# Kernel tuning notes

Measured on AMD Instinct MI355X. Metric: run time of the kernel, lower is better.

## Reference

```python
import jax, jax.numpy as jnp
import numpy as np

DIM = 384
WIN = 64
HEADS = 12
B_ = 4096


def setup_inputs() -> dict:
    key = jax.random.key(0)
    k1, k2, k3, k4, k5 = jax.random.split(key, 5)
    x = jax.random.normal(k1, (B_, WIN, DIM), dtype=jnp.float32)
    # torch Linear weights: qkv.weight [3*dim, dim], proj.weight [dim, dim], proj.bias [dim]
    qkv_w = jax.random.normal(k2, (3 * DIM, DIM), dtype=jnp.float32) * (DIM ** -0.5)
    proj_w = jax.random.normal(k3, (DIM, DIM), dtype=jnp.float32) * (DIM ** -0.5)
    proj_b = jax.random.normal(k4, (DIM,), dtype=jnp.float32) * 0.02
    bias_table = jax.random.normal(k5, (2 * WIN - 1, HEADS), dtype=jnp.float32) * 0.02
    return {"x": x, "qkv_w": qkv_w, "proj_w": proj_w, "proj_b": proj_b,
            "bias_table": bias_table}


def reference(x, qkv_w, proj_w, proj_b, bias_table):
    B, N, C = x.shape
    H = HEADS
    hd = C // H
    scale = hd ** -0.5
    # qkv projection (torch: x @ W.T), split into q,k,v [B,H,N,hd]
    qkv = jnp.einsum('bnc,dc->bnd', x, qkv_w)
    qkv = qkv.reshape(B, N, 3, H, hd).transpose(2, 0, 3, 1, 4)
    q, k, v = qkv[0] * scale, qkv[1], qkv[2]
    attn = jnp.einsum('bhnd,bhmd->bhnm', q, k)  # [B,H,N,N]
    # relative position bias: index [N,N] into table [2W-1,H]
    coords = jnp.arange(N)
    rel_idx = coords[:, None] - coords[None, :] + (N - 1)  # [N,N]
    bias = bias_table[rel_idx]  # [N,N,H]
    attn = attn + bias.transpose(2, 0, 1)[None]
    attn = jax.nn.softmax(attn, axis=-1)
    out = jnp.einsum('bhnm,bhmd->bhnd', attn, v)
    out = out.transpose(0, 2, 1, 3).reshape(B, N, C)
    out = jnp.einsum('bnc,dc->bnd', out, proj_w) + proj_b
    return out
```

## Files before the change

kernel.cpp:

```cpp
#include <hip/hip_runtime.h>
#include <stdint.h>

#define DIM 384
#define WIN 64
#define HEADS 12
#define HD 32
#define NWIN 4096

typedef _Float16 f16;
typedef unsigned int u32;
typedef _Float16 half8 __attribute__((ext_vector_type(8)));
typedef _Float16 half4 __attribute__((ext_vector_type(4)));
typedef float floatx4 __attribute__((ext_vector_type(4)));

#define AS1 __attribute__((address_space(1)))
#define AS3 __attribute__((address_space(3)))

__device__ __forceinline__ void gl_lds16(const void* g, void* l) {
    __builtin_amdgcn_global_load_lds((const AS1 u32*)g, (AS3 u32*)l, 16, 0, 0);
}

__global__ void cvt_kernel(const float* __restrict__ in, f16* __restrict__ out, long n4) {
    long i = (long)blockIdx.x * blockDim.x + threadIdx.x;
    const long stride = (long)gridDim.x * blockDim.x;
    for (; i < n4; i += stride) {
        float4 v = ((const float4*)in)[i];
        half4 h;
        h[0] = (f16)v.x; h[1] = (f16)v.y; h[2] = (f16)v.z; h[3] = (f16)v.w;
        ((half4*)out)[i] = h;
    }
}

__global__ void pack_w_kernel(const float* __restrict__ w, f16* __restrict__ Bp) {
    const int t = blockIdx.x * 256 + threadIdx.x;
    const int colb = t / 9216;
    const int r1 = t % 9216;
    const int s = r1 / 768;
    const int r2 = r1 % 768;
    const int kc = r2 / 192, u = r2 % 192;
    const float* sp = w + (size_t)(colb * 192 + u) * DIM + s * 32 + kc * 8;
    float4 a = *(const float4*)sp;
    float4 b = *(const float4*)(sp + 4);
    half8 o;
    o[0] = (f16)a.x; o[1] = (f16)a.y; o[2] = (f16)a.z; o[3] = (f16)a.w;
    o[4] = (f16)b.x; o[5] = (f16)b.y; o[6] = (f16)b.z; o[7] = (f16)b.w;
    *(half8*)(Bp + (size_t)t * 8) = o;
}

__global__ void pack_x_kernel(const float* __restrict__ x, f16* __restrict__ Xp) {
    const int b = blockIdx.x;
    const int s = b % 12;
    const int rowb = b / 12;
    const int t = threadIdx.x;
    const int kc = t & 3, rr = t >> 2;
#pragma unroll
    for (int h = 0; h < 2; ++h) {
        const int row = rr + h * 64;
        const float* sp = x + (size_t)(rowb * 128 + row) * DIM + s * 32 + kc * 8;
        float4 a = *(const float4*)sp;
        float4 bq = *(const float4*)(sp + 4);
        half8 o;
        o[0] = (f16)a.x;  o[1] = (f16)a.y;  o[2] = (f16)a.z;  o[3] = (f16)a.w;
        o[4] = (f16)bq.x; o[5] = (f16)bq.y; o[6] = (f16)bq.z; o[7] = (f16)bq.w;
        *(half8*)(Xp + ((size_t)b * 512 + kc * 128 + row) * 8) = o;
    }
}

__global__ void __launch_bounds__(512, 2)
qkv_kernel(const f16* __restrict__ Xp, const f16* __restrict__ Bp,
           f16* __restrict__ q_arr, f16* __restrict__ k_arr,
           f16* __restrict__ v_int, int nwg)
{
    __shared__ __align__(16) f16 ldsA[2][16384];
    __shared__ __align__(16) f16 ldsB[3][12288];

    int lin = blockIdx.x;
    int nlin = lin;
    if ((nwg & 7) == 0) nlin = (lin & 7) * (nwg >> 3) + (lin >> 3);
    const int colb = nlin % 6, rowb = nlin / 6;

    const int tid = threadIdx.x;
    const int wave = tid >> 6, lane = tid & 63;
    const int g = lane >> 4, c = lane & 15;
    const int wm = wave >> 1, wn = wave & 1;

    floatx4 acc[4][6] = {};

    auto stageA = [&](int t) {
        f16* da = &ldsA[t & 1][0];
#pragma unroll
        for (int r = 0; r < 4; ++r) {
            const int rg = r >> 1, ss = r & 1;
            const f16* src = Xp + ((size_t)(2 * rowb + rg) * 12 + (2 * t + ss)) * 4096
                             + (size_t)tid * 8;
            gl_lds16(src, da + r * 4096 + tid * 8);
        }
    };
    auto stageB = [&](int t) {
        f16* db = &ldsB[t % 3][0];
#pragma unroll
        for (int r = 0; r < 3; ++r) {
            const int ch = r * 512 + tid;
            const int ss = ch / 768, rem = ch % 768;
            const f16* src = Bp + ((size_t)colb * 12 + (2 * t + ss)) * 6144 + (size_t)rem * 8;
            gl_lds16(src, db + ch * 8);
        }
    };

    stageA(0); stageB(0); stageB(1);

#pragma unroll
    for (int t = 0; t < 6; ++t) {
        if (t < 5) asm volatile("s_waitcnt vmcnt(3)" ::: "memory");
        else       asm volatile("s_waitcnt vmcnt(0)" ::: "memory");
        __builtin_amdgcn_sched_barrier(0);
        __builtin_amdgcn_s_barrier();
        __builtin_amdgcn_sched_barrier(0);
        if (t < 5) stageA(t + 1);
        if (t < 4) stageB(t + 2);

        const f16* ab = &ldsA[t & 1][0];
        const f16* bb = &ldsB[t % 3][0];
#pragma unroll
        for (int ks = 0; ks < 2; ++ks) {
            half8 af[4], bf[6];
#pragma unroll
            for (int mi = 0; mi < 4; ++mi) {
                const int row = wm * 64 + mi * 16 + c;
                const int slab = (row >> 7) * 2 + ks;
                af[mi] = *(const half8*)(ab + slab * 4096 + g * 1024 + (row & 127) * 8);
            }
#pragma unroll
            for (int ni = 0; ni < 6; ++ni) {
                const int u = wn * 96 + ni * 16 + c;
                bf[ni] = *(const half8*)(bb + ks * 6144 + g * 1536 + u * 8);
            }
#pragma unroll
            for (int mi = 0; mi < 4; ++mi)
#pragma unroll
                for (int ni = 0; ni < 6; ++ni)
                    acc[mi][ni] = __builtin_amdgcn_mfma_f32_16x16x32_f16(
                        af[mi], bf[ni], acc[mi][ni], 0, 0, 0);
        }
    }

    const int which = colb >> 1;
    const int dbase = (colb & 1) * 192;
    const int b0 = rowb * 4 + wm;
    if (which < 2) {
        f16* dst = which ? k_arr : q_arr;
        const float sc = which ? 1.0f : 0.17677669529663687f;
#pragma unroll
        for (int ni = 0; ni < 6; ++ni) {
            const int d = dbase + wn * 96 + ni * 16 + c;
            const int h = d >> 5, e = d & 31;
            f16* base = dst + (size_t)(b0 * HEADS + h) * (WIN * HD) + e;
#pragma unroll
            for (int mi = 0; mi < 4; ++mi)
#pragma unroll
                for (int j = 0; j < 4; ++j) {
                    const int n = mi * 16 + g * 4 + j;
                    base[(size_t)n * HD] = (f16)(acc[mi][ni][j] * sc);
                }
        }
    } else {
#pragma unroll
        for (int ni = 0; ni < 6; ++ni) {
            const int d = dbase + wn * 96 + ni * 16 + c;
            const int h = d >> 5, e = d & 31;
            f16* vb = v_int + (size_t)(b0 * HEADS + h) * (WIN * HD);
#pragma unroll
            for (int mi = 0; mi < 4; ++mi) {
                const int n0 = mi * 16 + g * 4;
                half4 pk;
#pragma unroll
                for (int j = 0; j < 4; ++j) pk[j] = (f16)acc[mi][ni][j];
                *(half4*)(vb + (n0 >> 3) * 256 + e * 8 + (n0 & 7)) = pk;
            }
        }
    }
}

__global__ void proj_kernel(const f16* __restrict__ A, const f16* __restrict__ Bw,
                            float* __restrict__ outp, const float* __restrict__ proj_b,
                            int nwg)
{
    __shared__ __align__(16) f16 lds[3][2][4][128][8];

    int lin = blockIdx.x;
    int nlin = lin;
    if ((nwg & 7) == 0) nlin = (lin & 7) * (nwg >> 3) + (lin >> 3);
    const int colb = nlin % 3, rowb = nlin / 3;
    const int col0 = colb * 128, row0 = rowb * 128;

    const int tid = threadIdx.x;
    const int wave = tid >> 6, lane = tid & 63;
    const int g = lane >> 4, c = lane & 15;
    const int wm = wave >> 1, wn = wave & 1;

    floatx4 acc[4][4] = {};

    auto stage = [&](int t) {
        const int k0 = t * 32;
#pragma unroll
        for (int r = 0; r < 4; ++r) {
            const int u = wave + r * 4;
            const int isB = u >> 3;
            const int uu = u & 7;
            const int kc = uu >> 1, m0 = (uu & 1) * 64;
            const f16* src = (isB ? Bw + (size_t)(col0 + m0 + lane) * DIM
                                  : A  + (size_t)(row0 + m0 + lane) * DIM)
                             + k0 + kc * 8;
            gl_lds16(src, &lds[t % 3][isB][kc][m0][0]);
        }
    };

    stage(0); stage(1);

#pragma unroll
    for (int s = 0; s < 12; ++s) {
        if (s < 11) asm volatile("s_waitcnt vmcnt(4)" ::: "memory");
        else        asm volatile("s_waitcnt vmcnt(0)" ::: "memory");
        asm volatile("s_waitcnt lgkmcnt(0)" ::: "memory");
        __builtin_amdgcn_sched_barrier(0);
        __builtin_amdgcn_s_barrier();
        __builtin_amdgcn_sched_barrier(0);
        if (s < 10) stage(s + 2);

        half8 af[4], bf[4];
#pragma unroll
        for (int i = 0; i < 4; ++i) {
            af[i] = *(const half8*)&lds[s % 3][0][g][wm * 64 + i * 16 + c][0];
            bf[i] = *(const half8*)&lds[s % 3][1][g][wn * 64 + i * 16 + c][0];
        }
#pragma unroll
        for (int mi = 0; mi < 4; ++mi)
#pragma unroll
            for (int ni = 0; ni < 4; ++ni)
                acc[mi][ni] = __builtin_amdgcn_mfma_f32_16x16x32_f16(
                    af[mi], bf[ni], acc[mi][ni], 0, 0, 0);
    }

#pragma unroll
    for (int ni = 0; ni < 4; ++ni) {
        const int d = col0 + wn * 64 + ni * 16 + c;
        const float pb = proj_b[d];
#pragma unroll
        for (int mi = 0; mi < 4; ++mi)
#pragma unroll
            for (int j = 0; j < 4; ++j) {
                const size_t trow = (size_t)row0 + wm * 64 + mi * 16 + g * 4 + j;
                outp[trow * DIM + d] = acc[mi][ni][j] + pb;
            }
    }
}

__global__ void attn_kernel(const f16* __restrict__ q_arr, const f16* __restrict__ k_arr,
                            const f16* __restrict__ v_int,
                            const float* __restrict__ bias_table,
                            f16* __restrict__ attn_out)
{
    const int bid = blockIdx.x;
    const int bw = bid / HEADS, h = bid % HEADS;
    const f16* q = q_arr + (size_t)bid * (WIN * HD);
    const f16* k = k_arr + (size_t)bid * (WIN * HD);
    const f16* v = v_int + (size_t)bid * (WIN * HD);

    const int tid = threadIdx.x;
    const int w = tid >> 6, lane = tid & 63;
    const int g = lane >> 4, c = lane & 15;

    __shared__ float bias_lds[2 * WIN - 1];
    __shared__ __align__(16) f16 p_lds[8][64][8];

    for (int i = tid; i < 2 * WIN - 1; i += 256)
        bias_lds[i] = bias_table[(size_t)i * HEADS + h];
    __syncthreads();

    half8 qa = *(const half8*)(q + (16 * w + c) * HD + g * 8);
    floatx4 s[4];
#pragma unroll
    for (int t = 0; t < 4; ++t) {
        half8 kb = *(const half8*)(k + (16 * t + c) * HD + g * 8);
        floatx4 z = {};
        s[t] = __builtin_amdgcn_mfma_f32_16x16x32_f16(qa, kb, z, 0, 0, 0);
    }

    float pr[4][4];
#pragma unroll
    for (int j = 0; j < 4; ++j) {
        const int n = 16 * w + g * 4 + j;
        float mx = -1e30f;
#pragma unroll
        for (int t = 0; t < 4; ++t) {
            const int m = 16 * t + c;
            pr[j][t] = s[t][j] + bias_lds[n - m + 63];
            mx = fmaxf(mx, pr[j][t]);
        }
        mx = fmaxf(mx, __shfl_xor(mx, 1));
        mx = fmaxf(mx, __shfl_xor(mx, 2));
        mx = fmaxf(mx, __shfl_xor(mx, 4));
        mx = fmaxf(mx, __shfl_xor(mx, 8));
        float sum = 0.f;
#pragma unroll
        for (int t = 0; t < 4; ++t) { pr[j][t] = __expf(pr[j][t] - mx); sum += pr[j][t]; }
        sum += __shfl_xor(sum, 1);
        sum += __shfl_xor(sum, 2);
        sum += __shfl_xor(sum, 4);
        sum += __shfl_xor(sum, 8);
        const float r = 1.0f / sum;
#pragma unroll
        for (int t = 0; t < 4; ++t) {
            const int m = 16 * t + c;
            p_lds[m >> 3][n][m & 7] = (f16)(pr[j][t] * r);
        }
    }
    __syncthreads();

    half8 pa0 = *(const half8*)&p_lds[g][16 * w + c][0];
    half8 pa1 = *(const half8*)&p_lds[4 + g][16 * w + c][0];
    floatx4 o[2];
#pragma unroll
    for (int t = 0; t < 2; ++t) {
        half8 vb0 = *(const half8*)(v + g * 256 + (16 * t + c) * 8);
        half8 vb1 = *(const half8*)(v + (4 + g) * 256 + (16 * t + c) * 8);
        floatx4 z = {};
        o[t] = __builtin_amdgcn_mfma_f32_16x16x32_f16(pa0, vb0, z, 0, 0, 0);
        o[t] = __builtin_amdgcn_mfma_f32_16x16x32_f16(pa1, vb1, o[t], 0, 0, 0);
    }
#pragma unroll
    for (int t = 0; t < 2; ++t)
#pragma unroll
        for (int j = 0; j < 4; ++j) {
            const int n = 16 * w + g * 4 + j;
            attn_out[((size_t)bw * WIN + n) * DIM + h * HD + 16 * t + c] = (f16)o[t][j];
        }
}

extern "C" void kernel_launch(void* const* d_in, const int* in_sizes, int n_in,
                              void* d_out, int out_size, void* d_ws, size_t ws_size,
                              hipStream_t stream) {
    const float* x          = (const float*)d_in[0];
    const float* qkv_w      = (const float*)d_in[1];
    const float* proj_w     = (const float*)d_in[2];
    const float* proj_b     = (const float*)d_in[3];
    const float* bias_table = (const float*)d_in[4];
    float* out = (float*)d_out;
    (void)in_sizes; (void)n_in; (void)out_size;

    uintptr_t p = (uintptr_t)d_ws;
    auto carve = [&](size_t bytes) -> void* {
        uintptr_t q = p; p += (bytes + 255) & ~(size_t)255; return (void*)q;
    };
    f16* w16_proj = (f16*)carve((size_t)DIM * DIM * 2);
    f16* Bp       = (f16*)carve((size_t)6 * 12 * 768 * 8 * 2);
    const size_t fixed = p - (uintptr_t)d_ws;

    int CB = NWIN;
    while (CB > 16 && fixed + (size_t)CB * 245760 + 4096 > ws_size) CB >>= 1;

    f16* Xp = (f16*)carve((size_t)CB * WIN * DIM * 2);
    f16* qa = (f16*)carve((size_t)CB * HEADS * WIN * HD * 2);
    f16* ka = (f16*)carve((size_t)CB * HEADS * WIN * HD * 2);
    f16* vi = (f16*)carve((size_t)CB * HEADS * WIN * HD * 2);
    f16* ao = (f16*)carve((size_t)CB * WIN * DIM * 2);

    cvt_kernel<<<dim3(64), dim3(256), 0, stream>>>(proj_w, w16_proj, (long)(DIM * DIM / 4));
    pack_w_kernel<<<dim3(216), dim3(256), 0, stream>>>(qkv_w, Bp);

    for (int c0 = 0; c0 < NWIN; c0 += CB) {
        const float* xc = x + (size_t)c0 * WIN * DIM;
        const int rowbs = CB / 2;

        pack_x_kernel<<<dim3(rowbs * 12), dim3(256), 0, stream>>>(xc, Xp);

        const int nwg1 = (CB * WIN / 256) * 6;
        qkv_kernel<<<dim3(nwg1), dim3(512), 0, stream>>>(Xp, Bp, qa, ka, vi, nwg1);

        attn_kernel<<<dim3(CB * HEADS), dim3(256), 0, stream>>>(qa, ka, vi, bias_table, ao);

        const int nwg2 = rowbs * 3;
        proj_kernel<<<dim3(nwg2), dim3(256), 0, stream>>>(ao, w16_proj,
                                                          out + (size_t)c0 * WIN * DIM, proj_b, nwg2);
    }
}
```

Measured before the change: 915.7 us.

## Fuse x fp32-to-fp16 packing into QKV GEMM with register-staged prefetch

```diff
diff --git a/kernel.cpp b/kernel.cpp
--- a/kernel.cpp
+++ b/kernel.cpp
@@ -47,37 +47,19 @@
     *(half8*)(Bp + (size_t)t * 8) = o;
 }
 
-__global__ void pack_x_kernel(const float* __restrict__ x, f16* __restrict__ Xp) {
-    const int b = blockIdx.x;
-    const int s = b % 12;
-    const int rowb = b / 12;
-    const int t = threadIdx.x;
-    const int kc = t & 3, rr = t >> 2;
-#pragma unroll
-    for (int h = 0; h < 2; ++h) {
-        const int row = rr + h * 64;
-        const float* sp = x + (size_t)(rowb * 128 + row) * DIM + s * 32 + kc * 8;
-        float4 a = *(const float4*)sp;
-        float4 bq = *(const float4*)(sp + 4);
-        half8 o;
-        o[0] = (f16)a.x;  o[1] = (f16)a.y;  o[2] = (f16)a.z;  o[3] = (f16)a.w;
-        o[4] = (f16)bq.x; o[5] = (f16)bq.y; o[6] = (f16)bq.z; o[7] = (f16)bq.w;
-        *(half8*)(Xp + ((size_t)b * 512 + kc * 128 + row) * 8) = o;
-    }
-}
-
 __global__ void __launch_bounds__(512, 2)
-qkv_kernel(const f16* __restrict__ Xp, const f16* __restrict__ Bp,
+qkv_kernel(const float* __restrict__ X32, const f16* __restrict__ Bp,
            f16* __restrict__ q_arr, f16* __restrict__ k_arr,
            f16* __restrict__ v_int, int nwg)
 {
-    __shared__ __align__(16) f16 ldsA[2][16384];
+    __shared__ __align__(16) f16 xa[2][2][256][32];
     __shared__ __align__(16) f16 ldsB[3][12288];
 
     int lin = blockIdx.x;
     int nlin = lin;
     if ((nwg & 7) == 0) nlin = (lin & 7) * (nwg >> 3) + (lin >> 3);
     const int colb = nlin % 6, rowb = nlin / 6;
+    const int row0 = rowb * 256;
 
     const int tid = threadIdx.x;
     const int wave = tid >> 6, lane = tid & 63;
@@ -85,15 +67,27 @@
     const int wm = wave >> 1, wn = wave & 1;
 
     floatx4 acc[4][6] = {};
-
-    auto stageA = [&](int t) {
-        f16* da = &ldsA[t & 1][0];
-#pragma unroll
-        for (int r = 0; r < 4; ++r) {
-            const int rg = r >> 1, ss = r & 1;
-            const f16* src = Xp + ((size_t)(2 * rowb + rg) * 12 + (2 * t + ss)) * 4096
-                             + (size_t)tid * 8;
-            gl_lds16(src, da + r * 4096 + tid * 8);
+    float4 rA[8];
+
+    auto loadA = [&](int t) {
+#pragma unroll
+        for (int r = 0; r < 8; ++r) {
+            const int i = r * 512 + tid;
+            const int row = i >> 4, kq = i & 15;
+            rA[r] = *(const float4*)(X32 + (size_t)(row0 + row) * DIM + t * 64 + kq * 4);
+        }
+    };
+    auto writeA = [&](int t) {
+#pragma unroll
+        for (int r = 0; r < 8; ++r) {
+            const int i = r * 512 + tid;
+            const int row = i >> 4, kq = i & 15;
+            const int ks = kq >> 3, kq2 = kq & 7;
+            const int sl = (kq2 >> 1) ^ ((row >> 1) & 3);
+            half4 h;
+            h[0] = (f16)rA[r].x; h[1] = (f16)rA[r].y;
+            h[2] = (f16)rA[r].z; h[3] = (f16)rA[r].w;
+            *(half4*)&xa[t & 1][ks][row][sl * 8 + (kq2 & 1) * 4] = h;
         }
     };
     auto stageB = [&](int t) {
@@ -107,19 +101,19 @@
         }
     };
 
-    stageA(0); stageB(0); stageB(1);
+    loadA(0); stageB(0); stageB(1);
+    writeA(0);
+    loadA(1);
 
 #pragma unroll
     for (int t = 0; t < 6; ++t) {
-        if (t < 5) asm volatile("s_waitcnt vmcnt(3)" ::: "memory");
-        else       asm volatile("s_waitcnt vmcnt(0)" ::: "memory");
+        asm volatile("s_waitcnt vmcnt(11)" ::: "memory");
+        asm volatile("s_waitcnt lgkmcnt(0)" ::: "memory");
         __builtin_amdgcn_sched_barrier(0);
         __builtin_amdgcn_s_barrier();
         __builtin_amdgcn_sched_barrier(0);
-        if (t < 5) stageA(t + 1);
         if (t < 4) stageB(t + 2);
 
-        const f16* ab = &ldsA[t & 1][0];
         const f16* bb = &ldsB[t % 3][0];
 #pragma unroll
         for (int ks = 0; ks < 2; ++ks) {
@@ -127,8 +121,8 @@
 #pragma unroll
             for (int mi = 0; mi < 4; ++mi) {
                 const int row = wm * 64 + mi * 16 + c;
-                const int slab = (row >> 7) * 2 + ks;
-                af[mi] = *(const half8*)(ab + slab * 4096 + g * 1024 + (row & 127) * 8);
+                const int sl = g ^ ((row >> 1) & 3);
+                af[mi] = *(const half8*)&xa[t & 1][ks][row][sl * 8];
             }
 #pragma unroll
             for (int ni = 0; ni < 6; ++ni) {
@@ -142,6 +136,8 @@
                     acc[mi][ni] = __builtin_amdgcn_mfma_f32_16x16x32_f16(
                         af[mi], bf[ni], acc[mi][ni], 0, 0, 0);
         }
+        if (t < 5) writeA(t + 1);
+        if (t < 4) loadA(t + 2);
     }
 
     const int which = colb >> 1;
@@ -357,9 +353,8 @@
     const size_t fixed = p - (uintptr_t)d_ws;
 
     int CB = NWIN;
-    while (CB > 16 && fixed + (size_t)CB * 245760 + 4096 > ws_size) CB >>= 1;
-
-    f16* Xp = (f16*)carve((size_t)CB * WIN * DIM * 2);
+    while (CB > 16 && fixed + (size_t)CB * 196608 + 4096 > ws_size) CB >>= 1;
+
     f16* qa = (f16*)carve((size_t)CB * HEADS * WIN * HD * 2);
     f16* ka = (f16*)carve((size_t)CB * HEADS * WIN * HD * 2);
     f16* vi = (f16*)carve((size_t)CB * HEADS * WIN * HD * 2);
@@ -370,16 +365,13 @@
 
     for (int c0 = 0; c0 < NWIN; c0 += CB) {
         const float* xc = x + (size_t)c0 * WIN * DIM;
-        const int rowbs = CB / 2;
-
-        pack_x_kernel<<<dim3(rowbs * 12), dim3(256), 0, stream>>>(xc, Xp);
 
         const int nwg1 = (CB * WIN / 256) * 6;
-        qkv_kernel<<<dim3(nwg1), dim3(512), 0, stream>>>(Xp, Bp, qa, ka, vi, nwg1);
+        qkv_kernel<<<dim3(nwg1), dim3(512), 0, stream>>>(xc, Bp, qa, ka, vi, nwg1);
 
         attn_kernel<<<dim3(CB * HEADS), dim3(256), 0, stream>>>(qa, ka, vi, bias_table, ao);
 
-        const int nwg2 = rowbs * 3;
+        const int nwg2 = (CB * WIN / 128) * 3;
         proj_kernel<<<dim3(nwg2), dim3(256), 0, stream>>>(ao, w16_proj,
                                                           out + (size_t)c0 * WIN * DIM, proj_b, nwg2);
     }
```

Result: faster. 852.9 us (-6.9%).
